# Optimization experiments

Measured on AMD Instinct MI355X. Metric: run time of the kernel, lower is better.

## Reference

```python
import jax, jax.numpy as jnp
import numpy as np

N = 4096      # nnode
F = 128       # feature_dim
E = 64        # embed_dim
P_EDGE = 0.01 # edge probability (~41 avg degree)
NEG = -9e15
ALPHA = 0.2   # leaky relu slope


def _xavier(key, shape):
    lim = float(np.sqrt(6.0 / (shape[0] + shape[1])))
    return jax.random.uniform(key, shape, minval=-lim, maxval=lim, dtype=jnp.float32)


def setup_inputs() -> dict:
    key = jax.random.key(0)
    ks = jax.random.split(key, 14)
    features = jax.random.normal(ks[0], (N, F), dtype=jnp.float32)
    eye = jnp.eye(N, dtype=jnp.float32)

    def make_adj(k):
        a = (jax.random.uniform(k, (N, N)) < P_EDGE).astype(jnp.float32)
        return jnp.maximum(a, eye)  # self loop so no empty rows

    return {
        "features": features,
        "geo_adj": make_adj(ks[1]),
        "forward_adj": make_adj(ks[2]),
        "backward_adj": make_adj(ks[3]),
        "weight": _xavier(ks[4], (E, F)),
        "Wf": _xavier(ks[5], (F, E)),
        "af1": jax.random.normal(ks[6], (E,), dtype=jnp.float32) * 0.1,
        "af2": jax.random.normal(ks[7], (E,), dtype=jnp.float32) * 0.1,
        "Wb": _xavier(ks[8], (F, E)),
        "ab1": jax.random.normal(ks[9], (E,), dtype=jnp.float32) * 0.1,
        "ab2": jax.random.normal(ks[10], (E,), dtype=jnp.float32) * 0.1,
        "Wg": _xavier(ks[11], (F, E)),
        "ag1": jax.random.normal(ks[12], (E,), dtype=jnp.float32) * 0.1,
        "ag2": jax.random.normal(ks[13], (E,), dtype=jnp.float32) * 0.1,
    }


def _mean_neighbors(adj, feat):
    # pre_weight: row-normalized neighbor averaging, (N,N) @ (N,F)
    deg = jnp.clip(jnp.sum(adj, axis=1, keepdims=True), 1.0, None)
    return (adj @ feat) / deg


def _attention(feat, mask_feat, adj, W, a1, a2):
    # GAT-style additive attention with masked softmax over neighbors
    h = feat @ W        # (N, E)
    hm = mask_feat @ W  # (N, E)
    e = jax.nn.leaky_relu((h @ a1)[:, None] + (hm @ a2)[None, :], negative_slope=ALPHA)  # (N, N)
    e = jnp.where(adj > 0, e, NEG)
    return jax.nn.softmax(e, axis=1)  # (N, N)


def reference(features, geo_adj, forward_adj, backward_adj, weight,
              Wf, af1, af2, Wb, ab1, ab2, Wg, ag1, ag2):
    t = features  # (N, F)
    mask_f = _mean_neighbors(forward_adj, t)
    mask_b = _mean_neighbors(backward_adj, t)
    mask_g = _mean_neighbors(geo_adj, t)

    w_f = _attention(t, mask_f, forward_adj, Wf, af1, af2)
    w_b = _attention(t, mask_b, backward_adj, Wb, ab1, ab2)
    w_g = _attention(t, mask_g, geo_adj, Wg, ag1, ag2)

    # get_mask_matrix_i/_j broadcast-mul + sum(1) == attn @ t (or attn.T @ t)
    x = weight @ t.T                  # (E, N)
    x_fwd = weight @ (w_f @ t).T      # mask_matrix_i
    x_bwd = weight @ (w_b.T @ t).T    # mask_matrix_j (transposed)
    x_geo = weight @ (w_g @ t).T      # mask_matrix_i

    return jnp.concatenate([x, x_fwd, x_bwd, x_geo], axis=0)  # (4E, N)
```

## Files before the change

### kernel.cpp

```cpp
#include <hip/hip_runtime.h>

#define NN 4096
#define FF 128
#define EE 64

typedef unsigned short u16;
typedef unsigned long long u64;

__device__ __forceinline__ float lrelu(float x) { return x > 0.f ? x : 0.2f * x; }

__global__ void k_prep(const float* __restrict__ Wf, const float* __restrict__ af1, const float* __restrict__ af2,
                       const float* __restrict__ Wb, const float* __restrict__ ab1, const float* __restrict__ ab2,
                       const float* __restrict__ Wg, const float* __restrict__ ag1, const float* __restrict__ ag2,
                       float* __restrict__ v6)
{
    const float* Ws[3]  = {Wf, Wb, Wg};
    const float* a1s[3] = {af1, ab1, ag1};
    const float* a2s[3] = {af2, ab2, ag2};
    int tid = threadIdx.x;
    for (int idx = tid; idx < 6 * FF; idx += 256) {
        int vi = idx >> 7, f = idx & (FF - 1), dd = vi >> 1;
        const float* a = (vi & 1) ? a2s[dd] : a1s[dd];
        const float* W = Ws[dd];
        float s = 0.f;
        for (int e = 0; e < EE; ++e) s += W[(size_t)f * EE + e] * a[e];
        v6[idx] = s;
    }
}

__global__ void k_feat(const float* __restrict__ t, const float* __restrict__ weight,
                       const float* __restrict__ v6,
                       float* __restrict__ u, float* __restrict__ s1, float* __restrict__ p,
                       float* __restrict__ out, int* __restrict__ ccnt)
{
    __shared__ __attribute__((aligned(16))) float tt[FF];
    __shared__ float vv[6 * FF];
    int n = blockIdx.x, tid = threadIdx.x;
    if (n < 16) ccnt[n * 256 + tid] = 0;
    if (tid < FF) tt[tid] = t[(size_t)n * FF + tid];
    for (int idx = tid; idx < 6 * FF; idx += 256) vv[idx] = v6[idx];
    __syncthreads();
    int e = tid >> 2, part = tid & 3;
    const float4* w4 = reinterpret_cast<const float4*>(weight + (size_t)e * FF + part * 32);
    const float4* t4 = reinterpret_cast<const float4*>(tt + part * 32);
    float s = 0.f;
    #pragma unroll
    for (int q8 = 0; q8 < 8; ++q8) {
        float4 w = w4[q8]; float4 x = t4[q8];
        s += w.x * x.x + w.y * x.y + w.z * x.z + w.w * x.w;
    }
    s += __shfl_xor(s, 1); s += __shfl_xor(s, 2);
    if (part == 0) {
        u[(size_t)n * EE + e] = s;
        out[(size_t)e * NN + n] = s;
    }
    if (tid < 64) {
        float t0 = tt[tid], t1 = tt[64 + tid];
        for (int vi = 0; vi < 6; ++vi) {
            float x = t0 * vv[vi * FF + tid] + t1 * vv[vi * FF + 64 + tid];
            for (int off = 32; off; off >>= 1) x += __shfl_xor(x, off);
            if (tid == 0) {
                int dd = vi >> 1;
                if (vi & 1) p[dd * NN + n] = x; else s1[dd * NN + n] = x;
            }
        }
    }
}

__global__ __launch_bounds__(256, 4)
void k_mask(const float* __restrict__ Af, const float* __restrict__ Ab, const float* __restrict__ Ag,
            u64* __restrict__ masks)
{
    int wid = threadIdx.x >> 6, lane = threadIdx.x & 63;
    int wv = blockIdx.x * 4 + wid;
    int gr0 = wv * 4;
    int d = gr0 >> 12, r = gr0 & (NN - 1);
    const float* A = d == 0 ? Af : (d == 1 ? Ab : Ag);
    const float4* p0 = reinterpret_cast<const float4*>(A + (size_t)r * NN);
    const float4* p1 = p0 + 1024;
    const float4* p2 = p0 + 2048;
    const float4* p3 = p0 + 3072;
    u64 m0 = 0ull, m1 = 0ull, m2 = 0ull, m3 = 0ull;
    #pragma unroll
    for (int j = 0; j < 16; ++j) {
        float4 a = p0[j * 64 + lane];
        float4 b = p1[j * 64 + lane];
        float4 c = p2[j * 64 + lane];
        float4 e = p3[j * 64 + lane];
        int base = j * 4;
#define UPD(M, L) { u64 bx = __ballot(L.x != 0.f); u64 by = __ballot(L.y != 0.f); \
                    u64 bz = __ballot(L.z != 0.f); u64 bw = __ballot(L.w != 0.f); \
                    if (lane == base)     M = bx; \
                    if (lane == base + 1) M = by; \
                    if (lane == base + 2) M = bz; \
                    if (lane == base + 3) M = bw; }
        UPD(m0, a) UPD(m1, b) UPD(m2, c) UPD(m3, e)
#undef UPD
    }
    u64* mrow = masks + (size_t)gr0 * 64;
    mrow[lane] = m0;
    mrow[64 + lane] = m1;
    mrow[128 + lane] = m2;
    mrow[192 + lane] = m3;
}

__global__ void k_csr(const u64* __restrict__ masks, const float* __restrict__ p,
                      u16* __restrict__ csr, int* __restrict__ cnt, float* __restrict__ s2,
                      u16* __restrict__ csc, int* __restrict__ ccnt, int stride)
{
    int wid = threadIdx.x >> 6, lane = threadIdx.x & 63;
    int gr = blockIdx.x * 4 + wid;
    int d = gr >> 12, r = gr & (NN - 1);
    u64 m = masks[(size_t)gr * 64 + lane];
    int lc = __popcll(m);
    int sc = lc;
    for (int off = 1; off < 64; off <<= 1) {
        int o = __shfl_up(sc, off);
        if (lane >= off) sc += o;
    }
    int total = __shfl(sc, 63);
    int pos = sc - lc;
    const float* pd = p + d * NN;
    u16* crow = csr + (size_t)gr * stride;
    int colbase = (lane >> 2) * 256 + (lane & 3);
    float q = 0.f;
    while (m) {
        int b = __ffsll(m) - 1;
        m &= m - 1;
        int col = colbase + b * 4;
        if (pos < stride) crow[pos] = (u16)col;
        pos++;
        q += pd[col];
        if (d == 1) {
            int cp = atomicAdd(&ccnt[col], 1);
            if (cp < stride) csc[(size_t)col * stride + cp] = (u16)r;
        }
    }
    for (int off = 32; off; off >>= 1) q += __shfl_xor(q, off);
    if (lane == 0) {
        cnt[gr] = total;
        s2[gr] = q / fmaxf((float)total, 1.f);
    }
}

__global__ void k_zb(const float* __restrict__ s1, const float* __restrict__ s2,
                     const u16* __restrict__ csr, const int* __restrict__ cnt, int stride,
                     float* __restrict__ Zb)
{
    int tid = threadIdx.x, wave = tid >> 6, lane = tid & 63;
    int j = blockIdx.x * 4 + wave;
    int gr = NN + j;
    int nnz = min(cnt[gr], stride);
    const u16* crow = csr + (size_t)gr * stride;
    float s1j = s1[gr];
    const float* s2b = s2 + NN;
    float z = 0.f;
    if (lane < nnz)      z += __expf(lrelu(s1j + s2b[crow[lane]]));
    if (lane + 64 < nnz) z += __expf(lrelu(s1j + s2b[crow[lane + 64]]));
    for (int off = 32; off; off >>= 1) z += __shfl_xor(z, off);
    if (lane == 0) Zb[j] = z;
}

__global__ __launch_bounds__(256, 4)
void k_out(const float* __restrict__ u,
           const float* __restrict__ s1, const float* __restrict__ s2,
           const float* __restrict__ Zb,
           const u16* __restrict__ csr, const int* __restrict__ cnt,
           const u16* __restrict__ csc, const int* __restrict__ ccnt, int stride,
           float* __restrict__ out)
{
    int wid = threadIdx.x >> 6, lane = threadIdx.x & 63;
    int gr = blockIdx.x * 4 + wid;
    int d = gr >> 12, i = gr & (NN - 1);
    int nnz;
    int c0v = 0, c1v = 0;
    float w0v = 0.f, w1v = 0.f;
    if (d == 1) {
        nnz = min(ccnt[i], stride);
        const u16* cc = csc + (size_t)i * stride;
        float s2i = s2[NN + i];
        if (lane < nnz)      { int j = cc[lane];      c0v = j; w0v = __expf(lrelu(s1[NN + j] + s2i)) / Zb[j]; }
        if (lane + 64 < nnz) { int j = cc[lane + 64]; c1v = j; w1v = __expf(lrelu(s1[NN + j] + s2i)) / Zb[j]; }
    } else {
        nnz = min(cnt[gr], stride);
        const u16* crow = csr + (size_t)gr * stride;
        float s1i = s1[gr];
        const float* s2d = s2 + d * NN;
        float z = 0.f;
        if (lane < nnz)      { int c = crow[lane];      c0v = c; w0v = __expf(lrelu(s1i + s2d[c])); z += w0v; }
        if (lane + 64 < nnz) { int c = crow[lane + 64]; c1v = c; w1v = __expf(lrelu(s1i + s2d[c])); z += w1v; }
        for (int off = 32; off; off >>= 1) z += __shfl_xor(z, off);
        float invz = z > 0.f ? 1.f / z : 0.f;
        w0v *= invz; w1v *= invz;
    }
    float a0 = 0.f, a1 = 0.f;
    int n0 = nnz < 64 ? nnz : 64;
    int k = 0;
    for (; k + 1 < n0; k += 2) {
        int ca = __shfl(c0v, k), cb = __shfl(c0v, k + 1);
        float wa = __shfl(w0v, k), wb = __shfl(w0v, k + 1);
        a0 += wa * u[(size_t)ca * EE + lane];
        a1 += wb * u[(size_t)cb * EE + lane];
    }
    if (k < n0)
        a0 += __shfl(w0v, k) * u[(size_t)__shfl(c0v, k) * EE + lane];
    int n1 = nnz - 64;
    k = 0;
    for (; k + 1 < n1; k += 2) {
        int ca = __shfl(c1v, k), cb = __shfl(c1v, k + 1);
        float wa = __shfl(w1v, k), wb = __shfl(w1v, k + 1);
        a0 += wa * u[(size_t)ca * EE + lane];
        a1 += wb * u[(size_t)cb * EE + lane];
    }
    if (k < n1)
        a0 += __shfl(w1v, k) * u[(size_t)__shfl(c1v, k) * EE + lane];
    int base = 64 + (d << 6);
    out[(size_t)(base + lane) * NN + i] = a0 + a1;
}

extern "C" void kernel_launch(void* const* d_in, const int* in_sizes, int n_in,
                              void* d_out, int out_size, void* d_ws, size_t ws_size,
                              hipStream_t stream)
{
    const float* t   = (const float*)d_in[0];
    const float* Ag  = (const float*)d_in[1];
    const float* Af  = (const float*)d_in[2];
    const float* Ab  = (const float*)d_in[3];
    const float* W   = (const float*)d_in[4];
    const float* Wf  = (const float*)d_in[5];
    const float* af1 = (const float*)d_in[6];
    const float* af2 = (const float*)d_in[7];
    const float* Wb  = (const float*)d_in[8];
    const float* ab1 = (const float*)d_in[9];
    const float* ab2 = (const float*)d_in[10];
    const float* Wg  = (const float*)d_in[11];
    const float* ag1 = (const float*)d_in[12];
    const float* ag2 = (const float*)d_in[13];
    float* out = (float*)d_out;

    char* wsb = (char*)d_ws;
    u64*   masks = (u64*)wsb;
    float* v6  = (float*)(wsb + (size_t)3 * NN * 64 * 8);
    float* s1  = v6 + 6 * FF;
    float* p   = s1 + 3 * NN;
    float* s2  = p + 3 * NN;
    float* Zb  = s2 + 3 * NN;
    float* u   = Zb + NN;
    int*   cnt  = (int*)(u + (size_t)NN * EE);
    int*   ccnt = cnt + 3 * NN;
    u16*   csr  = (u16*)(ccnt + NN);

    size_t base_bytes = ((char*)csr) - wsb;
    int stride = 128;
    if (base_bytes + (size_t)4 * NN * 128 * 2 > ws_size) stride = 96;
    if (base_bytes + (size_t)4 * NN * 96 * 2 > ws_size)  stride = 64;
    u16* csc = csr + (size_t)3 * NN * stride;

    k_prep<<<1, 256, 0, stream>>>(Wf, af1, af2, Wb, ab1, ab2, Wg, ag1, ag2, v6);
    k_feat<<<NN, 256, 0, stream>>>(t, W, v6, u, s1, p, out, ccnt);
    k_mask<<<3 * NN / 16, 256, 0, stream>>>(Af, Ab, Ag, masks);
    k_csr<<<3 * NN / 4, 256, 0, stream>>>(masks, p, csr, cnt, s2, csc, ccnt, stride);
    k_zb<<<NN / 4, 256, 0, stream>>>(s1, s2, csr, cnt, stride, Zb);
    k_out<<<3 * NN / 4, 256, 0, stream>>>(u, s1, s2, Zb, csr, cnt, csc, ccnt, stride, out);
}
```

Measured before the change: 299.5 us.

## Fuse adjacency mask extraction into CSR build and parallelize prep kernel

Merges the mask-building kernel into the CSR construction kernel. Each wavefront now reads its adjacency row directly and builds a per-lane 64-bit mask with a new column mapping, so the intermediate bitmask buffer is no longer written to and read back from global memory and one launch goes away. The prep kernel is also spread over 6 blocks of 128 threads instead of a single block. In exchange, each wave now streams one row instead of four, and the CSR order within a row changes to lane-strided columns, which can alter the order of the floating-point summation.

New measurement: 269.9 us. 9.9% less time.

```diff
diff --git a/kernel.cpp b/kernel.cpp
--- a/kernel.cpp
+++ b/kernel.cpp
@@ -17,15 +17,13 @@
     const float* Ws[3]  = {Wf, Wb, Wg};
     const float* a1s[3] = {af1, ab1, ag1};
     const float* a2s[3] = {af2, ab2, ag2};
-    int tid = threadIdx.x;
-    for (int idx = tid; idx < 6 * FF; idx += 256) {
-        int vi = idx >> 7, f = idx & (FF - 1), dd = vi >> 1;
-        const float* a = (vi & 1) ? a2s[dd] : a1s[dd];
-        const float* W = Ws[dd];
-        float s = 0.f;
-        for (int e = 0; e < EE; ++e) s += W[(size_t)f * EE + e] * a[e];
-        v6[idx] = s;
-    }
+    int vi = blockIdx.x, f = threadIdx.x, dd = vi >> 1;
+    const float* a = (vi & 1) ? a2s[dd] : a1s[dd];
+    const float* W = Ws[dd] + (size_t)f * EE;
+    float s = 0.f;
+    #pragma unroll 8
+    for (int e = 0; e < EE; ++e) s += W[e] * a[e];
+    v6[vi * FF + f] = s;
 }
 
 __global__ void k_feat(const float* __restrict__ t, const float* __restrict__ weight,
@@ -68,51 +66,28 @@
 }
 
 __global__ __launch_bounds__(256, 4)
-void k_mask(const float* __restrict__ Af, const float* __restrict__ Ab, const float* __restrict__ Ag,
-            u64* __restrict__ masks)
-{
-    int wid = threadIdx.x >> 6, lane = threadIdx.x & 63;
-    int wv = blockIdx.x * 4 + wid;
-    int gr0 = wv * 4;
-    int d = gr0 >> 12, r = gr0 & (NN - 1);
-    const float* A = d == 0 ? Af : (d == 1 ? Ab : Ag);
-    const float4* p0 = reinterpret_cast<const float4*>(A + (size_t)r * NN);
-    const float4* p1 = p0 + 1024;
-    const float4* p2 = p0 + 2048;
-    const float4* p3 = p0 + 3072;
-    u64 m0 = 0ull, m1 = 0ull, m2 = 0ull, m3 = 0ull;
-    #pragma unroll
-    for (int j = 0; j < 16; ++j) {
-        float4 a = p0[j * 64 + lane];
-        float4 b = p1[j * 64 + lane];
-        float4 c = p2[j * 64 + lane];
-        float4 e = p3[j * 64 + lane];
-        int base = j * 4;
-#define UPD(M, L) { u64 bx = __ballot(L.x != 0.f); u64 by = __ballot(L.y != 0.f); \
-                    u64 bz = __ballot(L.z != 0.f); u64 bw = __ballot(L.w != 0.f); \
-                    if (lane == base)     M = bx; \
-                    if (lane == base + 1) M = by; \
-                    if (lane == base + 2) M = bz; \
-                    if (lane == base + 3) M = bw; }
-        UPD(m0, a) UPD(m1, b) UPD(m2, c) UPD(m3, e)
-#undef UPD
-    }
-    u64* mrow = masks + (size_t)gr0 * 64;
-    mrow[lane] = m0;
-    mrow[64 + lane] = m1;
-    mrow[128 + lane] = m2;
-    mrow[192 + lane] = m3;
-}
-
-__global__ void k_csr(const u64* __restrict__ masks, const float* __restrict__ p,
-                      u16* __restrict__ csr, int* __restrict__ cnt, float* __restrict__ s2,
-                      u16* __restrict__ csc, int* __restrict__ ccnt, int stride)
+void k_scan(const float* __restrict__ Af, const float* __restrict__ Ab, const float* __restrict__ Ag,
+            const float* __restrict__ p,
+            u16* __restrict__ csr, int* __restrict__ cnt, float* __restrict__ s2,
+            u16* __restrict__ csc, int* __restrict__ ccnt, int stride)
 {
     int wid = threadIdx.x >> 6, lane = threadIdx.x & 63;
     int gr = blockIdx.x * 4 + wid;
     int d = gr >> 12, r = gr & (NN - 1);
-    u64 m = masks[(size_t)gr * 64 + lane];
-    int lc = __popcll(m);
+    const float* A = d == 0 ? Af : (d == 1 ? Ab : Ag);
+    const float4* row4 = reinterpret_cast<const float4*>(A + (size_t)r * NN);
+    const float* pd = p + d * NN;
+
+    u64 mask = 0ull;
+    #pragma unroll
+    for (int j = 0; j < 16; ++j) {
+        float4 L = row4[j * 64 + lane];
+        unsigned mm = (L.x != 0.f ? 1u : 0u) | (L.y != 0.f ? 2u : 0u) |
+                      (L.z != 0.f ? 4u : 0u) | (L.w != 0.f ? 8u : 0u);
+        mask |= ((u64)mm) << (j * 4);
+    }
+
+    int lc = __popcll(mask);
     int sc = lc;
     for (int off = 1; off < 64; off <<= 1) {
         int o = __shfl_up(sc, off);
@@ -120,14 +95,13 @@
     }
     int total = __shfl(sc, 63);
     int pos = sc - lc;
-    const float* pd = p + d * NN;
     u16* crow = csr + (size_t)gr * stride;
-    int colbase = (lane >> 2) * 256 + (lane & 3);
     float q = 0.f;
+    u64 m = mask;
     while (m) {
         int b = __ffsll(m) - 1;
         m &= m - 1;
-        int col = colbase + b * 4;
+        int col = ((b >> 2) << 8) + (lane << 2) + (b & 3);
         if (pos < stride) crow[pos] = (u16)col;
         pos++;
         q += pd[col];
@@ -238,9 +212,8 @@
     const float* ag2 = (const float*)d_in[13];
     float* out = (float*)d_out;
 
-    char* wsb = (char*)d_ws;
-    u64*   masks = (u64*)wsb;
-    float* v6  = (float*)(wsb + (size_t)3 * NN * 64 * 8);
+    float* ws = (float*)d_ws;
+    float* v6  = ws;
     float* s1  = v6 + 6 * FF;
     float* p   = s1 + 3 * NN;
     float* s2  = p + 3 * NN;
@@ -250,16 +223,15 @@
     int*   ccnt = cnt + 3 * NN;
     u16*   csr  = (u16*)(ccnt + NN);
 
-    size_t base_bytes = ((char*)csr) - wsb;
+    size_t base_bytes = ((char*)csr) - ((char*)d_ws);
     int stride = 128;
     if (base_bytes + (size_t)4 * NN * 128 * 2 > ws_size) stride = 96;
     if (base_bytes + (size_t)4 * NN * 96 * 2 > ws_size)  stride = 64;
     u16* csc = csr + (size_t)3 * NN * stride;
 
-    k_prep<<<1, 256, 0, stream>>>(Wf, af1, af2, Wb, ab1, ab2, Wg, ag1, ag2, v6);
+    k_prep<<<6, 128, 0, stream>>>(Wf, af1, af2, Wb, ab1, ab2, Wg, ag1, ag2, v6);
     k_feat<<<NN, 256, 0, stream>>>(t, W, v6, u, s1, p, out, ccnt);
-    k_mask<<<3 * NN / 16, 256, 0, stream>>>(Af, Ab, Ag, masks);
-    k_csr<<<3 * NN / 4, 256, 0, stream>>>(masks, p, csr, cnt, s2, csc, ccnt, stride);
+    k_scan<<<3 * NN / 4, 256, 0, stream>>>(Af, Ab, Ag, p, csr, cnt, s2, csc, ccnt, stride);
     k_zb<<<NN / 4, 256, 0, stream>>>(s1, s2, csr, cnt, stride, Zb);
     k_out<<<3 * NN / 4, 256, 0, stream>>>(u, s1, s2, Zb, csr, cnt, csc, ccnt, stride, out);
 }
```
